# Optimization experiments

Hardware: AMD Instinct MI355X
Metric: run time of the kernel (lower is better)

## Reference

```python
import jax, jax.numpy as jnp
import numpy as np

B, L, C, S, W, R = 2, 32, 32, 64, 64, 32
MH = 32  # forcing MLP hidden


def _conv3d(x, w, b, pad_hw):
    # x: [B, Cin, L, S, W], w: [Cout, Cin, 1, kh, kw]
    y = jax.lax.conv_general_dilated(
        x, w, window_strides=(1, 1, 1),
        padding=[(0, 0), (pad_hw, pad_hw), (pad_hw, pad_hw)],
        dimension_numbers=('NCDHW', 'OIDHW', 'NCDHW'))
    return y + b[None, :, None, None, None]


def _forward(x, listT, params_log_base, dispersion_mod, fm_W1, fm_b1, fm_W2, fm_b2,
             forcing_scale, U_re, U_im, V_re, V_im, pW_re, pW_im, pb_re, pb_im,
             convr_w, convr_b, convi_w, convi_b, projc_w, projc_b, ln_w, ln_b):
    b, l, c, s, w = x.shape
    r = U_re.shape[-1]
    pad = s // 4
    dt = listT.reshape(b, l, 1, 1, 1)

    # FFT with mirror padding along S
    xp = jnp.pad(x, ((0, 0), (0, 0), (0, 0), (pad, pad), (0, 0)), mode='reflect')
    h = jnp.fft.fft2(xp.astype(jnp.complex64), axes=(-2, -1), norm='ortho')

    # complex channel projection
    proj_W = pW_re + 1j * pW_im
    h = jnp.einsum('blcsw,cd->bldsw', h, proj_W)
    h = h + (pb_re + 1j * pb_im)[None, None, :, None, None]

    # back to spatial, crop pad, re-FFT
    hs = jnp.fft.ifft2(h, axes=(-2, -1), norm='ortho')[..., pad:-pad, :]
    h = jnp.fft.fft2(hs, axes=(-2, -1), norm='ortho')

    U = U_re + 1j * U_im          # [C, S, R]
    V = V_re + 1j * V_im          # [C, W, R]
    # zq[b,l,c,r,q] = sum_{s,w} h * conj(U)[c,s,r] * V[c,w,q]
    zq = jnp.einsum('blcsw,csr,cwq->blcrq', h, jnp.conj(U), V)

    nu_base = jnp.exp(params_log_base[0] + dispersion_mod[0]).reshape(1, 1, c, r, 1)
    th_base = jnp.exp(params_log_base[1] + dispersion_mod[1]).reshape(1, 1, c, r, 1)

    # forcing modulation
    ctx = x.mean(axis=(-2, -1))                       # [B, L, C]
    inp = jnp.concatenate([ctx, dt.reshape(b, l, 1)], axis=-1)
    mid = jnp.tanh(inp @ fm_W1 + fm_b1)
    mod = (mid @ fm_W2 + fm_b2).reshape(b, l, c, r, 2)
    dnu = (forcing_scale * jnp.tanh(mod[..., 0]))[..., None]
    dth = (forcing_scale * jnp.tanh(mod[..., 1]))[..., None]

    nu_t = jnp.maximum(nu_base * dt + dnu, 1e-6)       # [B, L, C, R, 1]
    th_t = th_base * dt + dth
    lamb = jnp.exp(jax.lax.complex(-nu_t, th_t))       # complex [B, L, C, R, 1]

    gamma = jnp.sqrt(jnp.maximum(1.0 - jnp.exp(-2.0 * nu_t), 1e-12))
    x_in = zq * gamma.astype(zq.dtype)                 # [B, L, C, R, R]

    # parallel linear-recurrence scan: z_t = lamb_t * z_{t-1} + x_t
    def comb(a, bb):
        a1, x1 = a
        a2, x2 = bb
        return a1 * a2, a2 * x1 + x2
    _, z_out = jax.lax.associative_scan(comb, (lamb, x_in), axis=1)

    # reconstruct spectral field and inverse FFT
    h_rec = jnp.einsum('blcrq,cwq,csr->blcsw', z_out, jnp.conj(V), U)
    h_sp = jnp.fft.ifft2(h_rec, axes=(-2, -1), norm='ortho')

    xr = jnp.transpose(h_sp.real, (0, 2, 1, 3, 4))     # [B, C, L, S, W]
    xi = jnp.transpose(h_sp.imag, (0, 2, 1, 3, 4))
    hr = _conv3d(xr, convr_w, convr_b, 1)
    hi = _conv3d(xi, convi_w, convi_b, 1)
    hf = _conv3d(jnp.concatenate([hr, hi], axis=1), projc_w, projc_b, 0)
    hf = jnp.transpose(hf, (0, 2, 1, 3, 4))            # [B, L, C, S, W]

    # LayerNorm over [S, W]
    mu = hf.mean(axis=(-2, -1), keepdims=True)
    var = hf.var(axis=(-2, -1), keepdims=True)
    hf = (hf - mu) / jnp.sqrt(var + 1e-5) * ln_w + ln_b

    return x + hf


def setup_inputs() -> dict:
    key = jax.random.key(0)
    ks = jax.random.split(key, 20)
    f32 = jnp.float32
    x = jax.random.normal(ks[0], (B, L, C, S, W), dtype=f32)
    listT = jax.random.uniform(ks[1], (B, L), dtype=f32, minval=0.5, maxval=1.5)

    r_min, r_max = 0.8, 0.99
    u1 = jax.random.uniform(ks[2], (C, R), dtype=f32)
    u2 = jax.random.uniform(ks[3], (C, R), dtype=f32)
    nu_log = jnp.log(-0.5 * jnp.log(u1 * (r_max ** 2 - r_min ** 2) + r_min ** 2))
    theta_log = jnp.log(u2 * (2.0 * np.pi))
    params_log_base = jnp.stack([nu_log, theta_log], axis=0)
    dispersion_mod = jnp.zeros((2, C, R), dtype=f32)

    fm_W1 = jax.random.normal(ks[4], (C + 1, MH), dtype=f32) / np.sqrt(C + 1)
    fm_b1 = jnp.zeros((MH,), dtype=f32)
    fm_W2 = jax.random.normal(ks[5], (MH, C * R * 2), dtype=f32) / np.sqrt(MH)
    fm_b2 = jnp.zeros((C * R * 2,), dtype=f32)
    forcing_scale = jnp.float32(0.1)

    cplx_scale = 1.0 / np.sqrt(2.0)
    U_re = jax.random.normal(ks[6], (C, S, R), dtype=f32) * cplx_scale / np.sqrt(S)
    U_im = jax.random.normal(ks[7], (C, S, R), dtype=f32) * cplx_scale / np.sqrt(S)
    V_re = jax.random.normal(ks[8], (C, W, R), dtype=f32) * cplx_scale / np.sqrt(W)
    V_im = jax.random.normal(ks[9], (C, W, R), dtype=f32) * cplx_scale / np.sqrt(W)
    pW_re = jax.random.normal(ks[10], (C, C), dtype=f32) * cplx_scale / np.sqrt(C)
    pW_im = jax.random.normal(ks[11], (C, C), dtype=f32) * cplx_scale / np.sqrt(C)
    pb_re = jnp.zeros((C,), dtype=f32)
    pb_im = jnp.zeros((C,), dtype=f32)

    convr_w = jax.random.normal(ks[12], (C, C, 1, 3, 3), dtype=f32) * (1.0 / np.sqrt(C * 9))
    convr_b = jnp.zeros((C,), dtype=f32)
    convi_w = jax.random.normal(ks[13], (C, C, 1, 3, 3), dtype=f32) * (1.0 / np.sqrt(C * 9))
    convi_b = jnp.zeros((C,), dtype=f32)
    projc_w = jax.random.normal(ks[14], (C, 2 * C, 1, 1, 1), dtype=f32) * (1.0 / np.sqrt(2 * C))
    projc_b = jnp.zeros((C,), dtype=f32)

    ln_w = jnp.ones((S, W), dtype=f32)
    ln_b = jnp.zeros((S, W), dtype=f32)

    return dict(x=x, listT=listT, params_log_base=params_log_base,
                dispersion_mod=dispersion_mod, fm_W1=fm_W1, fm_b1=fm_b1,
                fm_W2=fm_W2, fm_b2=fm_b2, forcing_scale=forcing_scale,
                U_re=U_re, U_im=U_im, V_re=V_re, V_im=V_im,
                pW_re=pW_re, pW_im=pW_im, pb_re=pb_re, pb_im=pb_im,
                convr_w=convr_w, convr_b=convr_b, convi_w=convi_w, convi_b=convi_b,
                projc_w=projc_w, projc_b=projc_b, ln_w=ln_w, ln_b=ln_b)


def reference(x, listT, params_log_base, dispersion_mod, fm_W1, fm_b1, fm_W2, fm_b2,
              forcing_scale, U_re, U_im, V_re, V_im, pW_re, pW_im, pb_re, pb_im,
              convr_w, convr_b, convi_w, convi_b, projc_w, projc_b, ln_w, ln_b):
    return _forward(x, listT, params_log_base, dispersion_mod, fm_W1, fm_b1, fm_W2,
                    fm_b2, forcing_scale, U_re, U_im, V_re, V_im, pW_re, pW_im,
                    pb_re, pb_im, convr_w, convr_b, convi_w, convi_b, projc_w,
                    projc_b, ln_w, ln_b)
```

## Files before the change

kernel.cpp:

```cpp
#include <hip/hip_runtime.h>


typedef __attribute__((ext_vector_type(8))) short short8;
typedef __attribute__((ext_vector_type(4))) float floatx4;

__device__ __forceinline__ unsigned pack_bf16(float re, float im) {
  unsigned a = __float_as_uint(re), b = __float_as_uint(im);
  a = (a + 0x7FFFu + ((a >> 16) & 1u)) >> 16;
  b = (b + 0x7FFFu + ((b >> 16) & 1u)) >> 16;
  return a | (b << 16);
}
__device__ __forceinline__ unsigned short bf16r(float v) {
  unsigned a = __float_as_uint(v);
  return (unsigned short)((a + 0x7FFFu + ((a >> 16) & 1u)) >> 16);
}

__global__ __launch_bounds__(256) void k_mixprep(
    const float* __restrict__ x, const float* __restrict__ pWr,
    const float* __restrict__ pWi,
    const float* __restrict__ U_re, const float* __restrict__ U_im,
    const float* __restrict__ V_re, const float* __restrict__ V_im,
    const float* __restrict__ projc_w, const float* __restrict__ convr_w,
    const float* __restrict__ convi_w,
    unsigned* __restrict__ hs, float* __restrict__ ctxp,
    unsigned* __restrict__ zqA, unsigned* __restrict__ recA,
    unsigned* __restrict__ recB, unsigned* __restrict__ Wtb) {
  __shared__ __align__(16) char smem[33280];
  const int tid = threadIdx.x;
  if (blockIdx.x < 1024) {
    unsigned* xb_s = (unsigned*)smem;
    float(*red)[16][2] = (float(*)[16][2])(smem + 20480);
    unsigned* outb = (unsigned*)smem;
    const int bl = blockIdx.x >> 4;
    const int seg = blockIdx.x & 15;
    const int pxbase = seg * 256;
    const float* xb = x + (size_t)bl * 131072 + pxbase;
    float csa = 0.f, csb = 0.f;
#pragma unroll
    for (int t = 0; t < 4; ++t) {
      int i = t * 256 + tid;
      int c2 = i & 15, g4 = i >> 4;
      float4 a = *(const float4*)(xb + (2 * c2) * 4096 + g4 * 4);
      float4 b = *(const float4*)(xb + (2 * c2 + 1) * 4096 + g4 * 4);
      csa += a.x + a.y + a.z + a.w;
      csb += b.x + b.y + b.z + b.w;
#pragma unroll
      for (int j = 0; j < 4; ++j) {
        int px = g4 * 4 + j;
        xb_s[px * 20 + (((c2 >> 2) ^ (px & 3)) << 2) + (c2 & 3)] =
            pack_bf16(((const float*)&a)[j], ((const float*)&b)[j]);
      }
    }
    red[tid & 15][tid >> 4][0] = csa;
    red[tid & 15][tid >> 4][1] = csb;
    const int lane = tid & 63, wv = tid >> 6;
    const int qd = lane >> 4, ln = lane & 15;
    short8 arL, aiL, arH, aiH;
#pragma unroll
    for (int j = 0; j < 8; ++j) {
      int ci = qd * 8 + j;
      ((short*)&arL)[j] = (short)bf16r(pWr[ci * 32 + ln]);
      ((short*)&aiL)[j] = (short)bf16r(pWi[ci * 32 + ln]);
      ((short*)&arH)[j] = (short)bf16r(pWr[ci * 32 + 16 + ln]);
      ((short*)&aiH)[j] = (short)bf16r(pWi[ci * 32 + 16 + ln]);
    }
    __syncthreads();
    if (tid < 32) {
      int c2 = tid >> 1, part = tid & 1;
      float s = 0.f;
#pragma unroll
      for (int w = 0; w < 16; ++w) s += red[c2][w][part];
      ctxp[(bl * 16 + seg) * 32 + 2 * c2 + part] = s;
    }
    floatx4 RL[4], IL[4], RH[4], IH[4];
#pragma unroll
    for (int pt = 0; pt < 4; ++pt) {
      int pxt = wv * 4 + pt;
      int pxl = pxt * 16 + ln;
      short8 bfr = *(const short8*)&xb_s[pxl * 20 + ((qd ^ (pxl & 3)) << 2)];
      floatx4 z4 = {0.f, 0.f, 0.f, 0.f};
      RL[pt] = __builtin_amdgcn_mfma_f32_16x16x32_bf16(arL, bfr, z4, 0, 0, 0);
      IL[pt] = __builtin_amdgcn_mfma_f32_16x16x32_bf16(aiL, bfr, z4, 0, 0, 0);
      RH[pt] = __builtin_amdgcn_mfma_f32_16x16x32_bf16(arH, bfr, z4, 0, 0, 0);
      IH[pt] = __builtin_amdgcn_mfma_f32_16x16x32_bf16(aiH, bfr, z4, 0, 0, 0);
    }
    __syncthreads();
#pragma unroll
    for (int pt = 0; pt < 4; ++pt) {
      int px = (wv * 4 + pt) * 16 + ln;
#pragma unroll
      for (int j = 0; j < 4; ++j) {
        outb[(qd * 4 + j) * 260 + px] = pack_bf16(RL[pt][j], IL[pt][j]);
        outb[(16 + qd * 4 + j) * 260 + px] = pack_bf16(RH[pt][j], IH[pt][j]);
      }
    }
    __syncthreads();
    unsigned* ho = hs + (size_t)bl * 131072 + pxbase;
    const int px4 = tid & 63, dg = tid >> 6;
#pragma unroll
    for (int dd = 0; dd < 8; ++dd) {
      int d = dg * 8 + dd;
      uint4 v = *(const uint4*)&outb[d * 260 + px4 * 4];
      *(uint4*)(ho + d * 4096 + px4 * 4) = v;
    }
  } else if (blockIdx.x < 1088) {
    float2* A2 = (float2*)smem;
    float2* tw = (float2*)(smem + 16384);
    const int id = blockIdx.x - 1024;
    const int c = id >> 1, src = id & 1;
    const float* Ar = (src ? V_re : U_re) + c * 2048;
    const float* Ai = (src ? V_im : U_im) + c * 2048;
    if (tid < 64) {
      float sa, ca;
      sincosf((float)tid * 0.09817477042468103f, &sa, &ca);
      tw[tid] = make_float2(ca, sa);
    }
#pragma unroll
    for (int t = 0; t < 8; ++t) {
      int idx = t * 256 + tid;
      A2[idx] = make_float2(Ar[idx], Ai[idx]);
    }
    __syncthreads();
    const int kw = tid >> 2, mg = tid & 3;
    float sr[8] = {0.f, 0.f, 0.f, 0.f, 0.f, 0.f, 0.f, 0.f};
    float si[8] = {0.f, 0.f, 0.f, 0.f, 0.f, 0.f, 0.f, 0.f};
#pragma unroll 4
    for (int n = 0; n < 64; ++n) {
      float2 w = tw[(kw * n) & 63];
      float ws = src ? -w.y : w.y;
#pragma unroll
      for (int t4 = 0; t4 < 4; ++t4) {
        float4 p = *(const float4*)&A2[n * 32 + mg * 8 + t4 * 2];
        sr[2 * t4]     += p.x * w.x - p.y * ws;
        si[2 * t4]     += p.x * ws + p.y * w.x;
        sr[2 * t4 + 1] += p.z * w.x - p.w * ws;
        si[2 * t4 + 1] += p.z * ws + p.w * w.x;
      }
    }
#pragma unroll
    for (int j = 0; j < 8; ++j) {
      float r = sr[j] * 0.125f, i2 = si[j] * 0.125f;
      int m = mg * 8 + j;
      unsigned p_ri  = pack_bf16(r, i2);
      unsigned p_rmi = pack_bf16(r, -i2);
      unsigned p_ir  = pack_bf16(i2, r);
      unsigned p_mir = pack_bf16(-i2, r);
      if (src == 0) {
        zqA[((c * 4 + 2) * 32 + m) * 64 + kw] = p_ri;
        zqA[((c * 4 + 3) * 32 + m) * 64 + kw] = p_mir;
        recA[((c * 2 + 0) * 64 + kw) * 32 + m] = p_rmi;
        recA[((c * 2 + 1) * 64 + kw) * 32 + m] = p_ir;
      } else {
        zqA[((c * 4 + 0) * 32 + m) * 64 + kw] = p_rmi;
        zqA[((c * 4 + 1) * 32 + m) * 64 + kw] = p_ir;
        recB[((c * 2 + 0) * 64 + kw) * 32 + m] = p_ri;
        recB[((c * 2 + 1) * 64 + kw) * 32 + m] = p_mir;
      }
    }
  } else {
    int gid = (blockIdx.x - 1088) * 256 + tid;
    if (gid < 9216) {
      int co = gid / 288;
      int r2 = gid - co * 288;
      int tap = r2 >> 5, ci = r2 & 31;
      float sr = 0.f, si = 0.f;
      for (int m = 0; m < 32; ++m) {
        sr += projc_w[co * 64 + m]      * convr_w[(m * 32 + ci) * 9 + tap];
        si += projc_w[co * 64 + 32 + m] * convi_w[(m * 32 + ci) * 9 + tap];
      }
      Wtb[gid] = pack_bf16(sr, si);
    }
  }
}

__global__ __launch_bounds__(256) void k_zq(
    const unsigned* __restrict__ hs, const short* __restrict__ zqA,
    float2* __restrict__ zq,
    const float* __restrict__ ctxp, const float* __restrict__ listT,
    const float* __restrict__ plb, const float* __restrict__ dmod,
    const float* __restrict__ W1, const float* __restrict__ b1,
    const float* __restrict__ W2, const float* __restrict__ b2,
    const float* __restrict__ fscale,
    float2* __restrict__ lam, float* __restrict__ gam) {
  __shared__ unsigned HsB[4096];
  __shared__ unsigned T2[2048];
  __shared__ float mid_s[32];
  __shared__ float ctxs[32];
  const int tid = threadIdx.x;
  if (blockIdx.x >= 2048) {
    int bl = blockIdx.x - 2048;
    float dt = listT[bl];
    if (tid < 32) {
      float s = 0.f;
#pragma unroll
      for (int sg = 0; sg < 16; ++sg) s += ctxp[(bl * 16 + sg) * 32 + tid];
      ctxs[tid] = s * (1.f / 4096.f);
    }
    __syncthreads();
    if (tid < 32) {
      float a = b1[tid];
      for (int j = 0; j < 32; ++j) a += ctxs[j] * W1[j * 32 + tid];
      a += dt * W1[1024 + tid];
      mid_s[tid] = tanhf(a);
    }
    __syncthreads();
    float fs = fscale[0];
#pragma unroll
    for (int u = 0; u < 4; ++u) {
      int cr = u * 256 + tid;
      int col = cr * 2;
      float m0 = b2[col], m1 = b2[col + 1];
      for (int h = 0; h < 32; ++h) {
        float mh = mid_s[h];
        float2 w2 = *(const float2*)&W2[h * 2048 + col];
        m0 += mh * w2.x;
        m1 += mh * w2.y;
      }
      float dnu = fs * tanhf(m0);
      float dth = fs * tanhf(m1);
      float nub = expf(plb[cr] + dmod[cr]);
      float thb = expf(plb[1024 + cr] + dmod[1024 + cr]);
      float nut = fmaxf(nub * dt + dnu, 1e-6f);
      float tht = thb * dt + dth;
      float e = expf(-nut);
      float sa, ca;
      sincosf(tht, &sa, &ca);
      float g = sqrtf(fmaxf(1.f - expf(-2.f * nut), 1e-12f));
      int o = bl * 1024 + cr;
      lam[o] = make_float2(e * ca, e * sa);
      gam[o] = g;
    }
    return;
  }
  const int blc = blockIdx.x;
  const int c = blc & 31;
  const int lane = tid & 63, wv = tid >> 6;
  const int qd = lane >> 4, ln = lane & 15;
  const int mt = wv >> 1, nth = wv & 1;
  {
    const uint4* hp = (const uint4*)(hs + (size_t)blc * 4096);
#pragma unroll
    for (int it = 0; it < 4; ++it) {
      int i4 = tid + it * 256;
      uint4 v = hp[i4];
      int s = i4 >> 4, w4 = i4 & 15;
      *(uint4*)&HsB[s * 64 + ((w4 ^ (s & 15)) << 2)] = v;
    }
  }
  const short* zA = zqA + (size_t)c * 4 * 32 * 128;
  short8 a1[4], a2[4], a3[4], a4[4];
#pragma unroll
  for (int t = 0; t < 4; ++t) {
    int row = mt * 16 + ln;
    a1[t] = *(const short8*)(zA + (0 * 32 + row) * 128 + t * 32 + qd * 8);
    a2[t] = *(const short8*)(zA + (1 * 32 + row) * 128 + t * 32 + qd * 8);
    a3[t] = *(const short8*)(zA + (2 * 32 + row) * 128 + t * 32 + qd * 8);
    a4[t] = *(const short8*)(zA + (3 * 32 + row) * 128 + t * 32 + qd * 8);
  }
  __syncthreads();
#pragma unroll
  for (int nti = 0; nti < 2; ++nti) {
    int nt = nth * 2 + nti;
    int n = nt * 16 + ln;
    floatx4 accr = {0.f, 0.f, 0.f, 0.f}, acci = {0.f, 0.f, 0.f, 0.f};
#pragma unroll
    for (int t = 0; t < 4; ++t) {
      short8 b = *(const short8*)&HsB[n * 64 + (((4 * t + qd) ^ (n & 15)) << 2)];
      accr = __builtin_amdgcn_mfma_f32_16x16x32_bf16(a1[t], b, accr, 0, 0, 0);
      acci = __builtin_amdgcn_mfma_f32_16x16x32_bf16(a2[t], b, acci, 0, 0, 0);
    }
#pragma unroll
    for (int j = 0; j < 4; ++j) {
      int q = mt * 16 + qd * 4 + j;
      int s = n;
      T2[q * 64 + (((s >> 2) ^ (q & 15)) << 2) + (s & 3)] = pack_bf16(accr[j], acci[j]);
    }
  }
  __syncthreads();
  {
    const int mt2 = wv >> 1, nt2 = wv & 1;
    int n = nt2 * 16 + ln;
    floatx4 zr = {0.f, 0.f, 0.f, 0.f}, zi = {0.f, 0.f, 0.f, 0.f};
#pragma unroll
    for (int t = 0; t < 4; ++t) {
      short8 b = *(const short8*)&T2[n * 64 + (((4 * t + qd) ^ (n & 15)) << 2)];
      zr = __builtin_amdgcn_mfma_f32_16x16x32_bf16(a3[t], b, zr, 0, 0, 0);
      zi = __builtin_amdgcn_mfma_f32_16x16x32_bf16(a4[t], b, zi, 0, 0, 0);
    }
    float2* zo = zq + (size_t)blc * 1024;
#pragma unroll
    for (int j = 0; j < 4; ++j) {
      int r = mt2 * 16 + qd * 4 + j;
      zo[r * 32 + n] = make_float2(zr[j], zi[j]);
    }
  }
}

__global__ __launch_bounds__(256) void k_scan(const float2* __restrict__ lam,
                                              const float* __restrict__ gam,
                                              const float2* __restrict__ zin,
                                              unsigned* __restrict__ zsp,
                                              int zst) {
  __shared__ float2 se[4][64];
  __shared__ float2 pe[4][64];
  __shared__ float2 cr_s[4][64];
  const int bc = blockIdx.x >> 4;
  const int b = bc >> 5, c = bc & 31;
  const int rq0 = (blockIdx.x & 15) * 64;
  const int seg = threadIdx.x >> 6, u = threadIdx.x & 63;
  const int rq = rq0 + u, r = rq >> 5;
  const int t0 = seg * 8;
  float2 s = make_float2(0.f, 0.f), P = make_float2(1.f, 0.f);
  float2 zloc[8], Ps[8];
  float2 v = zin[((size_t)(b * 32 + t0) * 32 + c) * 1024 + rq];
  float2 lm = lam[(b * 32 + t0) * 1024 + c * 32 + r];
  float g = gam[(b * 32 + t0) * 1024 + c * 32 + r];
#pragma unroll
  for (int i = 0; i < 8; ++i) {
    float2 nv, nlm;
    float ng;
    if (i < 7) {
      int t = t0 + i + 1;
      nv = zin[((size_t)(b * 32 + t) * 32 + c) * 1024 + rq];
      nlm = lam[(b * 32 + t) * 1024 + c * 32 + r];
      ng = gam[(b * 32 + t) * 1024 + c * 32 + r];
    }
    float nr = lm.x * s.x - lm.y * s.y + g * v.x;
    float ni = lm.x * s.y + lm.y * s.x + g * v.y;
    s = make_float2(nr, ni);
    float pr = P.x * lm.x - P.y * lm.y;
    float pi = P.x * lm.y + P.y * lm.x;
    P = make_float2(pr, pi);
    zloc[i] = s;
    Ps[i] = P;
    v = nv; lm = nlm; g = ng;
  }
  se[seg][u] = s;
  pe[seg][u] = P;
  __syncthreads();
  if (threadIdx.x < 64) {
    float2 c1 = se[0][u];
    float2 p1 = pe[1][u], s1 = se[1][u];
    float2 c2 = make_float2(s1.x + p1.x * c1.x - p1.y * c1.y,
                            s1.y + p1.x * c1.y + p1.y * c1.x);
    float2 p2 = pe[2][u], s2 = se[2][u];
    float2 c3 = make_float2(s2.x + p2.x * c2.x - p2.y * c2.y,
                            s2.y + p2.x * c2.y + p2.y * c2.x);
    cr_s[0][u] = make_float2(0.f, 0.f);
    cr_s[1][u] = c1;
    cr_s[2][u] = c2;
    cr_s[3][u] = c3;
  }
  __syncthreads();
  float2 cr = cr_s[seg][u];
#pragma unroll
  for (int i = 0; i < 8; ++i) {
    float zr = zloc[i].x + Ps[i].x * cr.x - Ps[i].y * cr.y;
    float zi = zloc[i].y + Ps[i].x * cr.y + Ps[i].y * cr.x;
    size_t idx = ((size_t)(b * 32 + t0 + i) * 32 + c) * 1024 + rq;
    zsp[idx * zst] = pack_bf16(zr, zi);
  }
}

__global__ __launch_bounds__(256) void k_rec(const unsigned* __restrict__ zs,
                                             int zst,
                                             const short* __restrict__ recA,
                                             const short* __restrict__ recB,
                                             unsigned* __restrict__ hsp) {
  __shared__ unsigned zB[1024];
  __shared__ unsigned P[2048];
  const int blc = blockIdx.x;
  const int c = blc & 31;
  const int tid = threadIdx.x;
  const int lane = tid & 63, wv = tid >> 6;
  const int qd = lane >> 4, ln = lane & 15;
  {
    const unsigned* zp = zs + (size_t)blc * 1024 * zst;
#pragma unroll
    for (int it = 0; it < 4; ++it) {
      int i = tid + it * 256;
      unsigned pv = zp[(size_t)i * zst];
      int r = i >> 5, q = i & 31;
      zB[q * 32 + (((r >> 2) ^ (q & 7)) << 2) + (r & 3)] = pv;
    }
  }
  const short* rA = recA + (size_t)c * 2 * 64 * 64;
  short8 a5[2], a6[2];
#pragma unroll
  for (int t = 0; t < 2; ++t) {
    int row = wv * 16 + ln;
    a5[t] = *(const short8*)(rA + (0 * 64 + row) * 64 + t * 32 + qd * 8);
    a6[t] = *(const short8*)(rA + (1 * 64 + row) * 64 + t * 32 + qd * 8);
  }
  __syncthreads();
#pragma unroll
  for (int nt = 0; nt < 2; ++nt) {
    int n = nt * 16 + ln;
    floatx4 pr = {0.f, 0.f, 0.f, 0.f}, pi = {0.f, 0.f, 0.f, 0.f};
#pragma unroll
    for (int t = 0; t < 2; ++t) {
      short8 b = *(const short8*)&zB[n * 32 + (((4 * t + qd) ^ (n & 7)) << 2)];
      pr = __builtin_amdgcn_mfma_f32_16x16x32_bf16(a5[t], b, pr, 0, 0, 0);
      pi = __builtin_amdgcn_mfma_f32_16x16x32_bf16(a6[t], b, pi, 0, 0, 0);
    }
#pragma unroll
    for (int j = 0; j < 4; ++j) {
      int s = wv * 16 + qd * 4 + j;
      int q = n;
      P[s * 32 + (((q >> 2) ^ (s & 7)) << 2) + (q & 3)] = pack_bf16(pr[j], pi[j]);
    }
  }
  __syncthreads();
  const short* rB = recB + (size_t)c * 2 * 64 * 64;
  short8 pa[2];
#pragma unroll
  for (int t = 0; t < 2; ++t) {
    int row = wv * 16 + ln;
    pa[t] = *(const short8*)&P[row * 32 + (((4 * t + qd) ^ (row & 7)) << 2)];
  }
#pragma unroll
  for (int nt = 0; nt < 4; ++nt) {
    int n = nt * 16 + ln;
    floatx4 hr = {0.f, 0.f, 0.f, 0.f}, hi = {0.f, 0.f, 0.f, 0.f};
#pragma unroll
    for (int t = 0; t < 2; ++t) {
      short8 b5 = *(const short8*)(rB + (0 * 64 + n) * 64 + t * 32 + qd * 8);
      short8 b6 = *(const short8*)(rB + (1 * 64 + n) * 64 + t * 32 + qd * 8);
      hr = __builtin_amdgcn_mfma_f32_16x16x32_bf16(pa[t], b5, hr, 0, 0, 0);
      hi = __builtin_amdgcn_mfma_f32_16x16x32_bf16(pa[t], b6, hi, 0, 0, 0);
    }
    unsigned* ho = hsp + (size_t)blc * 4096;
#pragma unroll
    for (int j = 0; j < 4; ++j) {
      int s = wv * 16 + qd * 4 + j;
      ho[s * 64 + n] = pack_bf16(hr[j], hi[j]);
    }
  }
}

__global__ __launch_bounds__(256, 2) void k_conv(
    const unsigned* __restrict__ hsp, const short* __restrict__ Wtb,
    unsigned short* __restrict__ convout, float2* __restrict__ stats) {
  __shared__ unsigned lds_in[6 * 66 * 32];
  const int bl = blockIdx.x >> 4;
  const int slab = blockIdx.x & 15;
  const int y0 = slab * 4;
  const int tid = threadIdx.x;
  for (int i = tid; i < 384; i += 256) {
    int ci = i & 31, j = i >> 5;
    int yi = j >> 1, xi = (j & 1) ? 65 : 0;
    int slot = (ci >> 2) ^ (xi & 7);
    lds_in[(yi * 66 + xi) * 32 + slot * 4 + (ci & 3)] = 0u;
  }
#pragma unroll
  for (int t = 0; t < 12; ++t) {
    int i = t * 256 + tid;
    int ci = i & 31;
    int j = i >> 5;
    int yi = j >> 4, x4 = j & 15;
    int y = y0 + yi - 1;
    uint4 v = make_uint4(0u, 0u, 0u, 0u);
    if ((unsigned)y < 64u)
      v = *(const uint4*)(hsp + (((size_t)bl * 32 + ci) * 64 + y) * 64 + x4 * 4);
    int xb = 1 + x4 * 4;
#pragma unroll
    for (int jj = 0; jj < 4; ++jj) {
      int xi = xb + jj;
      int slot = (ci >> 2) ^ (xi & 7);
      lds_in[(yi * 66 + xi) * 32 + slot * 4 + (ci & 3)] =
          ((const unsigned*)&v)[jj];
    }
  }
  const int lane = tid & 63;
  const int wv = tid >> 6;
  const int co = lane & 15;
  const int qd = lane >> 4;
  short8 bL[18], bH[18];
  {
    const short* wpL = Wtb + (co * 9) * 64 + qd * 8;
    const short* wpH = Wtb + ((co + 16) * 9) * 64 + qd * 8;
#pragma unroll
    for (int tap = 0; tap < 9; ++tap)
#pragma unroll
      for (int kk = 0; kk < 2; ++kk) {
        bL[tap * 2 + kk] = *(const short8*)(wpL + tap * 64 + kk * 32);
        bH[tap * 2 + kk] = *(const short8*)(wpH + tap * 64 + kk * 32);
      }
  }
  __syncthreads();
  float sL = 0.f, s2L = 0.f, sH = 0.f, s2H = 0.f;
  const int x0 = wv * 16;
  const int xl = lane & 15;
  for (int ry = 0; ry < 4; ++ry) {
    floatx4 aL = {0.f, 0.f, 0.f, 0.f}, aH = {0.f, 0.f, 0.f, 0.f};
#pragma unroll
    for (int tap = 0; tap < 9; ++tap) {
      int dy = tap / 3, dx = tap - dy * 3;
      int yi = ry + dy;
      int xi = x0 + xl + dx;
#pragma unroll
      for (int kk = 0; kk < 2; ++kk) {
        int slot = ((kk << 2) | qd) ^ (xi & 7);
        const short8 a =
            *(const short8*)&lds_in[(yi * 66 + xi) * 32 + slot * 4];
        aL = __builtin_amdgcn_mfma_f32_16x16x32_bf16(a, bL[tap * 2 + kk], aL, 0, 0, 0);
        aH = __builtin_amdgcn_mfma_f32_16x16x32_bf16(a, bH[tap * 2 + kk], aH, 0, 0, 0);
      }
    }
    size_t goL = (((size_t)bl * 32 + co) * 64 + (y0 + ry)) * 64 + x0 + qd * 4;
    size_t goH = goL + (size_t)16 * 4096;
    *(uint2*)(convout + goL) =
        make_uint2(pack_bf16(aL[0], aL[1]), pack_bf16(aL[2], aL[3]));
    *(uint2*)(convout + goH) =
        make_uint2(pack_bf16(aH[0], aH[1]), pack_bf16(aH[2], aH[3]));
#pragma unroll
    for (int j = 0; j < 4; ++j) {
      sL += aL[j]; s2L += aL[j] * aL[j];
      sH += aH[j]; s2H += aH[j] * aH[j];
    }
  }
  sL += __shfl_down(sL, 32, 64);  s2L += __shfl_down(s2L, 32, 64);
  sH += __shfl_down(sH, 32, 64);  s2H += __shfl_down(s2H, 32, 64);
  sL += __shfl_down(sL, 16, 64);  s2L += __shfl_down(s2L, 16, 64);
  sH += __shfl_down(sH, 16, 64);  s2H += __shfl_down(s2H, 16, 64);
  if (lane < 16) {
    stats[((size_t)bl * 32 + lane) * 64 + slab * 4 + wv] = make_float2(sL, s2L);
    stats[((size_t)bl * 32 + 16 + lane) * 64 + slab * 4 + wv] =
        make_float2(sH, s2H);
  }
}

__global__ __launch_bounds__(256) void k_ln(
    const unsigned short* __restrict__ convout,
    const float2* __restrict__ stats, const float* __restrict__ x,
    const float* __restrict__ ln_w, const float* __restrict__ ln_b,
    float* __restrict__ out) {
  const int blc = blockIdx.x;
  const int tid = threadIdx.x;
  __shared__ float sh_mu, sh_rs;
  if (tid < 64) {
    float2 v = stats[(size_t)blc * 64 + tid];
    float s = v.x, s2 = v.y;
#pragma unroll
    for (int o = 32; o > 0; o >>= 1) {
      s += __shfl_down(s, o, 64);
      s2 += __shfl_down(s2, o, 64);
    }
    if (tid == 0) {
      float mu = s * (1.f / 4096.f);
      float var = s2 * (1.f / 4096.f) - mu * mu;
      sh_mu = mu;
      sh_rs = rsqrtf(var + 1e-5f);
    }
  }
  __syncthreads();
  float mu = sh_mu, rs = sh_rs;
  const uint2* cp = (const uint2*)(convout + (size_t)blc * 4096);
  const float4* xp = (const float4*)(x + (size_t)blc * 4096);
  const float4* lwp = (const float4*)ln_w;
  const float4* lbp = (const float4*)ln_b;
  float4* op = (float4*)(out + (size_t)blc * 4096);
#pragma unroll
  for (int k = 0; k < 4; ++k) {
    int i = tid + k * 256;
    uint2 cv = cp[i];
    float4 xv = xp[i], lw = lwp[i], lb = lbp[i];
    float c0 = __uint_as_float(cv.x << 16);
    float c1 = __uint_as_float(cv.x & 0xFFFF0000u);
    float c2 = __uint_as_float(cv.y << 16);
    float c3 = __uint_as_float(cv.y & 0xFFFF0000u);
    float4 o;
    o.x = xv.x + (c0 - mu) * rs * lw.x + lb.x;
    o.y = xv.y + (c1 - mu) * rs * lw.y + lb.y;
    o.z = xv.z + (c2 - mu) * rs * lw.z + lb.z;
    o.w = xv.w + (c3 - mu) * rs * lw.w + lb.w;
    op[i] = o;
  }
}

extern "C" void kernel_launch(void* const* d_in, const int* in_sizes, int n_in,
                              void* d_out, int out_size, void* d_ws,
                              size_t ws_size, hipStream_t stream) {
  const float* x       = (const float*)d_in[0];
  const float* listT   = (const float*)d_in[1];
  const float* plb     = (const float*)d_in[2];
  const float* dmod    = (const float*)d_in[3];
  const float* fm_W1   = (const float*)d_in[4];
  const float* fm_b1   = (const float*)d_in[5];
  const float* fm_W2   = (const float*)d_in[6];
  const float* fm_b2   = (const float*)d_in[7];
  const float* fscale  = (const float*)d_in[8];
  const float* U_re    = (const float*)d_in[9];
  const float* U_im    = (const float*)d_in[10];
  const float* V_re    = (const float*)d_in[11];
  const float* V_im    = (const float*)d_in[12];
  const float* pW_re   = (const float*)d_in[13];
  const float* pW_im   = (const float*)d_in[14];
  const float* convr_w = (const float*)d_in[17];
  const float* convi_w = (const float*)d_in[19];
  const float* projc_w = (const float*)d_in[21];
  const float* ln_w    = (const float*)d_in[23];
  const float* ln_b    = (const float*)d_in[24];
  float* out = (float*)d_out;

  float* wsf = (float*)d_ws;
  unsigned* hs  = (unsigned*)wsf;
  unsigned* hsp = (unsigned*)wsf;
  unsigned* zqAp  = (unsigned*)(wsf + 8388608);
  unsigned* recAp = (unsigned*)(wsf + 8388608 + 262144);
  unsigned* recBp = (unsigned*)(wsf + 8388608 + 393216);
  unsigned short* convout = (unsigned short*)(wsf + 8388608);
  float2*   stats = (float2*)(wsf + 12582912);
  float2*   zq  = (float2*)(wsf + 16777216);
  size_t off = 16777216 + 4194304;
  const size_t tail = 238592;
  unsigned* zs;
  int zst;
  size_t off2;
  if (ws_size >= (off + 2097152 + tail) * 4) {
    zs = (unsigned*)(wsf + off); zst = 1; off2 = off + 2097152;
  } else {
    zs = (unsigned*)zq; zst = 2; off2 = off;
  }
  float2*   lam  = (float2*)(wsf + off2);
  float*    gam  = wsf + off2 + 131072;
  float*    ctxp = wsf + off2 + 196608;
  unsigned* Wtb  = (unsigned*)(wsf + off2 + 229376);

  k_mixprep<<<1124, 256, 0, stream>>>(x, pW_re, pW_im, U_re, U_im, V_re, V_im,
                                      projc_w, convr_w, convi_w, hs, ctxp,
                                      zqAp, recAp, recBp, Wtb);
  k_zq<<<2112, 256, 0, stream>>>(hs, (const short*)zqAp, zq, ctxp, listT, plb,
                                 dmod, fm_W1, fm_b1, fm_W2, fm_b2, fscale,
                                 lam, gam);
  k_scan<<<1024, 256, 0, stream>>>(lam, gam, zq, zs, zst);
  k_rec<<<2048, 256, 0, stream>>>(zs, zst, (const short*)recAp,
                                  (const short*)recBp, hsp);
  k_conv<<<1024, 256, 0, stream>>>(hsp, (const short*)Wtb, convout, stats);
  k_ln<<<2048, 256, 0, stream>>>(convout, stats, x, ln_w, ln_b, out);
}
```

Before: 240.2 us.

## Fuse conv and layernorm kernels via per-group atomic barrier; batch scan loads

Merges the conv and layernorm kernels into one launch. The 16 slab blocks of each (b,l) group signal an atomic counter and spin until all 16 have written their partial stats, then each block normalizes two channels. This removes a kernel launch and the boundary between the two kernels. It relies on all 16 blocks of a group being co-resident, which the 1024-block grid with 2 blocks per CU should satisfy on this GPU, but spinning can stall, and a memset is added. The scan kernel also issues all eight time-step loads up front instead of software-prefetching one step ahead.

```diff
diff --git a/kernel.cpp b/kernel.cpp
--- a/kernel.cpp
+++ b/kernel.cpp
@@ -130,11 +130,11 @@
       float ws = src ? -w.y : w.y;
 #pragma unroll
       for (int t4 = 0; t4 < 4; ++t4) {
-        float4 p = *(const float4*)&A2[n * 32 + mg * 8 + t4 * 2];
-        sr[2 * t4]     += p.x * w.x - p.y * ws;
-        si[2 * t4]     += p.x * ws + p.y * w.x;
-        sr[2 * t4 + 1] += p.z * w.x - p.w * ws;
-        si[2 * t4 + 1] += p.z * ws + p.w * w.x;
+        float4 q = *(const float4*)&A2[n * 32 + mg * 8 + t4 * 2];
+        sr[2 * t4]     += q.x * w.x - q.y * ws;
+        si[2 * t4]     += q.x * ws + q.y * w.x;
+        sr[2 * t4 + 1] += q.z * w.x - q.w * ws;
+        si[2 * t4 + 1] += q.z * ws + q.w * w.x;
       }
     }
 #pragma unroll
@@ -310,30 +310,28 @@
   const int seg = threadIdx.x >> 6, u = threadIdx.x & 63;
   const int rq = rq0 + u, r = rq >> 5;
   const int t0 = seg * 8;
+  float2 vv[8], ll[8];
+  float gg[8];
+#pragma unroll
+  for (int i = 0; i < 8; ++i) {
+    int t = b * 32 + t0 + i;
+    vv[i] = zin[((size_t)t * 32 + c) * 1024 + rq];
+    ll[i] = lam[t * 1024 + c * 32 + r];
+    gg[i] = gam[t * 1024 + c * 32 + r];
+  }
   float2 s = make_float2(0.f, 0.f), P = make_float2(1.f, 0.f);
   float2 zloc[8], Ps[8];
-  float2 v = zin[((size_t)(b * 32 + t0) * 32 + c) * 1024 + rq];
-  float2 lm = lam[(b * 32 + t0) * 1024 + c * 32 + r];
-  float g = gam[(b * 32 + t0) * 1024 + c * 32 + r];
 #pragma unroll
   for (int i = 0; i < 8; ++i) {
-    float2 nv, nlm;
-    float ng;
-    if (i < 7) {
-      int t = t0 + i + 1;
-      nv = zin[((size_t)(b * 32 + t) * 32 + c) * 1024 + rq];
-      nlm = lam[(b * 32 + t) * 1024 + c * 32 + r];
-      ng = gam[(b * 32 + t) * 1024 + c * 32 + r];
-    }
-    float nr = lm.x * s.x - lm.y * s.y + g * v.x;
-    float ni = lm.x * s.y + lm.y * s.x + g * v.y;
+    float2 lm = ll[i];
+    float nr = lm.x * s.x - lm.y * s.y + gg[i] * vv[i].x;
+    float ni = lm.x * s.y + lm.y * s.x + gg[i] * vv[i].y;
     s = make_float2(nr, ni);
     float pr = P.x * lm.x - P.y * lm.y;
     float pi = P.x * lm.y + P.y * lm.x;
     P = make_float2(pr, pi);
     zloc[i] = s;
     Ps[i] = P;
-    v = nv; lm = nlm; g = ng;
   }
   se[seg][u] = s;
   pe[seg][u] = P;
@@ -438,10 +436,14 @@
   }
 }
 
-__global__ __launch_bounds__(256, 2) void k_conv(
+__global__ __launch_bounds__(256, 2) void k_convln(
     const unsigned* __restrict__ hsp, const short* __restrict__ Wtb,
-    unsigned short* __restrict__ convout, float2* __restrict__ stats) {
+    const float* __restrict__ x, const float* __restrict__ ln_w,
+    const float* __restrict__ ln_b, unsigned short* __restrict__ convout,
+    float2* __restrict__ stats, int* __restrict__ done,
+    float* __restrict__ out) {
   __shared__ unsigned lds_in[6 * 66 * 32];
+  __shared__ float sh_mu[2], sh_rs[2];
   const int bl = blockIdx.x >> 4;
   const int slab = blockIdx.x & 15;
   const int y0 = slab * 4;
@@ -528,53 +530,61 @@
     stats[((size_t)bl * 32 + 16 + lane) * 64 + slab * 4 + wv] =
         make_float2(sH, s2H);
   }
-}
-
-__global__ __launch_bounds__(256) void k_ln(
-    const unsigned short* __restrict__ convout,
-    const float2* __restrict__ stats, const float* __restrict__ x,
-    const float* __restrict__ ln_w, const float* __restrict__ ln_b,
-    float* __restrict__ out) {
-  const int blc = blockIdx.x;
-  const int tid = threadIdx.x;
-  __shared__ float sh_mu, sh_rs;
-  if (tid < 64) {
-    float2 v = stats[(size_t)blc * 64 + tid];
-    float s = v.x, s2 = v.y;
-#pragma unroll
-    for (int o = 32; o > 0; o >>= 1) {
-      s += __shfl_down(s, o, 64);
-      s2 += __shfl_down(s2, o, 64);
-    }
-    if (tid == 0) {
-      float mu = s * (1.f / 4096.f);
-      float var = s2 * (1.f / 4096.f) - mu * mu;
-      sh_mu = mu;
-      sh_rs = rsqrtf(var + 1e-5f);
-    }
-  }
-  __syncthreads();
-  float mu = sh_mu, rs = sh_rs;
-  const uint2* cp = (const uint2*)(convout + (size_t)blc * 4096);
-  const float4* xp = (const float4*)(x + (size_t)blc * 4096);
-  const float4* lwp = (const float4*)ln_w;
-  const float4* lbp = (const float4*)ln_b;
-  float4* op = (float4*)(out + (size_t)blc * 4096);
-#pragma unroll
-  for (int k = 0; k < 4; ++k) {
-    int i = tid + k * 256;
-    uint2 cv = cp[i];
-    float4 xv = xp[i], lw = lwp[i], lb = lbp[i];
-    float c0 = __uint_as_float(cv.x << 16);
-    float c1 = __uint_as_float(cv.x & 0xFFFF0000u);
-    float c2 = __uint_as_float(cv.y << 16);
-    float c3 = __uint_as_float(cv.y & 0xFFFF0000u);
-    float4 o;
-    o.x = xv.x + (c0 - mu) * rs * lw.x + lb.x;
-    o.y = xv.y + (c1 - mu) * rs * lw.y + lb.y;
-    o.z = xv.z + (c2 - mu) * rs * lw.z + lb.z;
-    o.w = xv.w + (c3 - mu) * rs * lw.w + lb.w;
-    op[i] = o;
+  __threadfence();
+  __syncthreads();
+  if (tid == 0) {
+    __hip_atomic_fetch_add(&done[bl], 1, __ATOMIC_RELEASE,
+                           __HIP_MEMORY_SCOPE_AGENT);
+    while (__hip_atomic_load(&done[bl], __ATOMIC_ACQUIRE,
+                             __HIP_MEMORY_SCOPE_AGENT) < 16)
+      __builtin_amdgcn_s_sleep(2);
+  }
+  __syncthreads();
+#pragma unroll
+  for (int half = 0; half < 2; ++half) {
+    const int blc = bl * 32 + slab * 2 + half;
+    if (tid < 64) {
+      float2 v = stats[(size_t)blc * 64 + tid];
+      float s = v.x, s2 = v.y;
+#pragma unroll
+      for (int o = 32; o > 0; o >>= 1) {
+        s += __shfl_down(s, o, 64);
+        s2 += __shfl_down(s2, o, 64);
+      }
+      if (tid == 0) {
+        float mu = s * (1.f / 4096.f);
+        float var = s2 * (1.f / 4096.f) - mu * mu;
+        sh_mu[half] = mu;
+        sh_rs[half] = rsqrtf(var + 1e-5f);
+      }
+    }
+  }
+  __syncthreads();
+#pragma unroll
+  for (int half = 0; half < 2; ++half) {
+    const int blc = bl * 32 + slab * 2 + half;
+    const float mu = sh_mu[half], rs = sh_rs[half];
+    const uint2* cp = (const uint2*)(convout + (size_t)blc * 4096);
+    const float4* xp = (const float4*)(x + (size_t)blc * 4096);
+    const float4* lwp = (const float4*)ln_w;
+    const float4* lbp = (const float4*)ln_b;
+    float4* op = (float4*)(out + (size_t)blc * 4096);
+#pragma unroll
+    for (int k = 0; k < 4; ++k) {
+      int i = tid + k * 256;
+      uint2 cv = cp[i];
+      float4 xv = xp[i], lw = lwp[i], lb = lbp[i];
+      float c0 = __uint_as_float(cv.x << 16);
+      float c1 = __uint_as_float(cv.x & 0xFFFF0000u);
+      float c2 = __uint_as_float(cv.y << 16);
+      float c3 = __uint_as_float(cv.y & 0xFFFF0000u);
+      float4 o;
+      o.x = xv.x + (c0 - mu) * rs * lw.x + lb.x;
+      o.y = xv.y + (c1 - mu) * rs * lw.y + lb.y;
+      o.z = xv.z + (c2 - mu) * rs * lw.z + lb.z;
+      o.w = xv.w + (c3 - mu) * rs * lw.w + lb.w;
+      op[i] = o;
+    }
   }
 }
 
@@ -613,7 +623,7 @@
   float2*   stats = (float2*)(wsf + 12582912);
   float2*   zq  = (float2*)(wsf + 16777216);
   size_t off = 16777216 + 4194304;
-  const size_t tail = 238592;
+  const size_t tail = 238720;
   unsigned* zs;
   int zst;
   size_t off2;
@@ -626,7 +636,9 @@
   float*    gam  = wsf + off2 + 131072;
   float*    ctxp = wsf + off2 + 196608;
   unsigned* Wtb  = (unsigned*)(wsf + off2 + 229376);
-
+  int*      done = (int*)(wsf + off2 + 238592);
+
+  hipMemsetAsync(done, 0, 256, stream);
   k_mixprep<<<1124, 256, 0, stream>>>(x, pW_re, pW_im, U_re, U_im, V_re, V_im,
                                       projc_w, convr_w, convi_w, hs, ctxp,
                                       zqAp, recAp, recBp, Wtb);
@@ -636,6 +648,6 @@
   k_scan<<<1024, 256, 0, stream>>>(lam, gam, zq, zs, zst);
   k_rec<<<2048, 256, 0, stream>>>(zs, zst, (const short*)recAp,
                                   (const short*)recBp, hsp);
-  k_conv<<<1024, 256, 0, stream>>>(hsp, (const short*)Wtb, convout, stats);
-  k_ln<<<2048, 256, 0, stream>>>(convout, stats, x, ln_w, ln_b, out);
-}
+  k_convln<<<1024, 256, 0, stream>>>(hsp, (const short*)Wtb, x, ln_w, ln_b,
+                                     convout, stats, done, out);
+}
```

Result: slower. 465.9 us (+93.9%).
